# Optimization experiments

Measured on AMD Instinct MI355X. Metric: run time of the kernel, lower is better.

## Reference

```python
import jax, jax.numpy as jnp
import numpy as np

NUM_HEADS = 32
KV_HEADS = 8
HEAD_DIM = 64
HIDDEN = 2048
ROPE_THETA = 10000.0


def setup_inputs() -> dict:
    key = jax.random.key(0)
    ks = jax.random.split(key, 5)
    B, S, H = 2, 2048, HIDDEN
    scale = 0.02
    return {
        "x": jax.random.normal(ks[0], (B, S, H), dtype=jnp.float32),
        # weights stored as (in_features, out_features)
        "Wq": jax.random.normal(ks[1], (H, NUM_HEADS * HEAD_DIM), dtype=jnp.float32) * scale,
        "Wk": jax.random.normal(ks[2], (H, KV_HEADS * HEAD_DIM), dtype=jnp.float32) * scale,
        "Wv": jax.random.normal(ks[3], (H, KV_HEADS * HEAD_DIM), dtype=jnp.float32) * scale,
        "Wo": jax.random.normal(ks[4], (H, H), dtype=jnp.float32) * scale,
    }


def _rope_tables(seq_len, dtype):
    # freq over even dims, angles concatenated twice -> (S, HEAD_DIM)
    freq = 1.0 / (ROPE_THETA ** (jnp.arange(0, HEAD_DIM, 2, dtype=jnp.float32) / HEAD_DIM))
    ang = jnp.arange(seq_len, dtype=jnp.float32)[:, None] * freq[None, :]
    emb = jnp.concatenate([ang, ang], axis=-1)
    return jnp.cos(emb).astype(dtype), jnp.sin(emb).astype(dtype)


def _rotate_half(x):
    x1, x2 = jnp.split(x, 2, axis=-1)
    return jnp.concatenate([-x2, x1], axis=-1)


def reference(x, Wq, Wk, Wv, Wo):
    B, S, H = x.shape
    q = jnp.einsum("bsd,df->bsf", x, Wq).reshape(B, S, NUM_HEADS, HEAD_DIM).transpose(0, 2, 1, 3)
    k = jnp.einsum("bsd,df->bsf", x, Wk).reshape(B, S, KV_HEADS, HEAD_DIM).transpose(0, 2, 1, 3)
    v = jnp.einsum("bsd,df->bsf", x, Wv).reshape(B, S, KV_HEADS, HEAD_DIM).transpose(0, 2, 1, 3)

    cos, sin = _rope_tables(S, x.dtype)  # (S, HEAD_DIM), broadcasts over (B, h, S, D)
    q = q * cos + _rotate_half(q) * sin
    k = k * cos + _rotate_half(k) * sin

    n_rep = NUM_HEADS // KV_HEADS
    k = jnp.repeat(k, n_rep, axis=1)  # (B, NUM_HEADS, S, D)
    v = jnp.repeat(v, n_rep, axis=1)

    scores = jnp.einsum("bhsd,bhtd->bhst", q, k) / jnp.sqrt(jnp.asarray(HEAD_DIM, x.dtype))
    weights = jax.nn.softmax(scores, axis=-1)
    ctx = jnp.einsum("bhst,bhtd->bhsd", weights, v)
    ctx = ctx.transpose(0, 2, 1, 3).reshape(B, S, H)
    return jnp.einsum("bsd,df->bsf", ctx, Wo)
```

## Files before the change

kernel.cpp:

```cpp
#include <hip/hip_runtime.h>

typedef short s8v __attribute__((ext_vector_type(8)));
typedef int i2v __attribute__((ext_vector_type(2)));
typedef float f4v __attribute__((ext_vector_type(4)));

typedef const __attribute__((address_space(1))) char* gp1_t;
typedef __attribute__((address_space(3))) char* lp3_t;

__device__ __forceinline__ float bf2f(short s) {
    union { unsigned u; float f; } c;
    c.u = ((unsigned)(unsigned short)s) << 16;
    return c.f;
}
__device__ __forceinline__ short f2bf(float f) {
    union { float f; unsigned u; } c; c.f = f;
    unsigned r = (c.u + 0x7FFFu + ((c.u >> 16) & 1u)) >> 16;
    return (short)r;
}
__device__ __forceinline__ unsigned cvt_pk_bf16(float a, float b) {
    unsigned r;
    asm("v_cvt_pk_bf16_f32 %0, %1, %2" : "=v"(r) : "v"(a), "v"(b));
    return r;
}
__device__ __forceinline__ s8v cvt8(const float* __restrict__ p) {
    f4v a = *(const f4v*)p;
    f4v b = *(const f4v*)(p + 4);
    s8v r;
    r[0] = f2bf(a[0]); r[1] = f2bf(a[1]); r[2] = f2bf(a[2]); r[3] = f2bf(a[3]);
    r[4] = f2bf(b[0]); r[5] = f2bf(b[1]); r[6] = f2bf(b[2]); r[7] = f2bf(b[3]);
    return r;
}


__global__ __launch_bounds__(256) void cvt_x(const float* __restrict__ x,
                                             short* __restrict__ xb) {
    long i = ((long)blockIdx.x * 256 + threadIdx.x) * 8;
    *(s8v*)&xb[i] = cvt8(&x[i]);
}

__global__ __launch_bounds__(256) void cvt_wt(const float* __restrict__ W,
                                              short* __restrict__ Wt,
                                              int N, int obase) {
    __shared__ __align__(16) short tile[64 * 72];
    const int kt = blockIdx.y * 64, n0 = blockIdx.x * 64;
    const int t = threadIdx.x;
    const int r = t >> 4, c4 = (t & 15) * 4;
#pragma unroll
    for (int i = 0; i < 4; i++) {
        int kr = r + i * 16;
        f4v v = *(const f4v*)&W[(long)(kt + kr) * N + n0 + c4];
#pragma unroll
        for (int j = 0; j < 4; j++) tile[(c4 + j) * 72 + kr] = f2bf(v[j]);
    }
    __syncthreads();
    const int nr = t >> 3, kc = (t & 7) * 8;
#pragma unroll
    for (int i = 0; i < 2; i++) {
        int n = nr + i * 32;
        *(s8v*)&Wt[(long)(obase + n0 + n) * 2048 + kt + kc] = *(const s8v*)&tile[n * 72 + kc];
    }
}

template <bool CF32>
__global__ __launch_bounds__(256) void gemm_bt(const short* __restrict__ A,
                                               const short* __restrict__ Bt,
                                               void* __restrict__ Cv,
                                               int K, int lda, int ldb, int ldc) {
    __shared__ __align__(16) short As[128 * 32];
    __shared__ __align__(16) short Bs[128 * 32];
    const int tid = threadIdx.x;
    const int lane = tid & 63;
    const int wave = tid >> 6;
    const int quad = lane >> 4;
    const int l15 = lane & 15;
    const int m0 = blockIdx.y * 128;
    const int n0 = blockIdx.x * 128;
    const int wm = (wave & 1) * 64;
    const int wn = (wave >> 1) * 64;

    f4v acc[4][4];
#pragma unroll
    for (int i = 0; i < 4; i++)
#pragma unroll
        for (int j = 0; j < 4; j++) acc[i][j] = (f4v){0.f, 0.f, 0.f, 0.f};

    const int s0 = wave * 64 + lane, s1 = (4 + wave) * 64 + lane;
    const short* a0 = A + (long)(m0 + (s0 >> 2)) * lda + (s0 & 3) * 8;
    const short* a1 = A + (long)(m0 + (s1 >> 2)) * lda + (s1 & 3) * 8;
    const short* b0 = Bt + (long)(n0 + (s0 >> 2)) * ldb + (s0 & 3) * 8;
    const short* b1 = Bt + (long)(n0 + (s1 >> 2)) * ldb + (s1 & 3) * 8;
    char* lA0 = (char*)As + wave * 1024;
    char* lA1 = (char*)As + (4 + wave) * 1024;
    char* lB0 = (char*)Bs + wave * 1024;
    char* lB1 = (char*)Bs + (4 + wave) * 1024;

    for (int k0 = 0; k0 < K; k0 += 32) {
        __syncthreads();
        __builtin_amdgcn_global_load_lds((gp1_t)(a0 + k0), (lp3_t)lA0, 16, 0, 0);
        __builtin_amdgcn_global_load_lds((gp1_t)(a1 + k0), (lp3_t)lA1, 16, 0, 0);
        __builtin_amdgcn_global_load_lds((gp1_t)(b0 + k0), (lp3_t)lB0, 16, 0, 0);
        __builtin_amdgcn_global_load_lds((gp1_t)(b1 + k0), (lp3_t)lB1, 16, 0, 0);
        __syncthreads();
        s8v af[4], bfr[4];
#pragma unroll
        for (int mi = 0; mi < 4; mi++)
            af[mi] = *(const s8v*)(&As[(wm + mi * 16 + l15) * 32 + quad * 8]);
#pragma unroll
        for (int ni = 0; ni < 4; ni++)
            bfr[ni] = *(const s8v*)(&Bs[(wn + ni * 16 + l15) * 32 + quad * 8]);
#pragma unroll
        for (int mi = 0; mi < 4; mi++)
#pragma unroll
            for (int ni = 0; ni < 4; ni++)
                acc[mi][ni] = __builtin_amdgcn_mfma_f32_16x16x32_bf16(af[mi], bfr[ni], acc[mi][ni], 0, 0, 0);
    }
#pragma unroll
    for (int mi = 0; mi < 4; mi++)
#pragma unroll
        for (int ni = 0; ni < 4; ni++)
#pragma unroll
            for (int r = 0; r < 4; r++) {
                int row = m0 + wm + mi * 16 + quad * 4 + r;
                int col = n0 + wn + ni * 16 + l15;
                if (CF32) ((float*)Cv)[(long)row * ldc + col] = acc[mi][ni][r];
                else      ((short*)Cv)[(long)row * ldc + col] = f2bf(acc[mi][ni][r]);
            }
}

__global__ __launch_bounds__(256) void rope_kernel(short* __restrict__ qkv) {
    int tid = blockIdx.x * 256 + threadIdx.x;
    int p = tid % 1280;
    int row = tid / 1280;
    int head = p >> 5;
    int j = p & 31;
    int s = row & 2047;
    int c1 = head * 64 + j;
    float freq = exp2f(-(float)j * 0.4152410118609203f);
    float ang = (float)s * freq;
    float sn, cs;
    __sincosf(ang, &sn, &cs);
    long base = (long)row * 3072;
    float x1 = bf2f(qkv[base + c1]);
    float x2 = bf2f(qkv[base + c1 + 32]);
    qkv[base + c1]      = f2bf(x1 * cs - x2 * sn);
    qkv[base + c1 + 32] = f2bf(x2 * cs + x1 * sn);
}

__global__ __launch_bounds__(256) void vtrans(const short* __restrict__ qkv,
                                              short* __restrict__ Vt_g) {
    __shared__ __align__(16) short tile[64 * 72];
    const int kt = blockIdx.x * 64;
    const int kvh = blockIdx.y;
    const int b = blockIdx.z;
    const int t = threadIdx.x;
#pragma unroll
    for (int cc = 0; cc < 2; cc++) {
        int ch = t + cc * 256;
        int key = ch >> 3, d0 = (ch & 7) * 8;
        s8v v = *(const s8v*)&qkv[(long)(b * 2048 + kt + key) * 3072 + 2560 + kvh * 64 + d0];
#pragma unroll
        for (int i = 0; i < 8; i++) tile[(d0 + i) * 72 + key] = v[i];
    }
    __syncthreads();
#pragma unroll
    for (int cc = 0; cc < 2; cc++) {
        int ch = t + cc * 256;
        int d = ch >> 3, kc = (ch & 7) * 8;
        *(s8v*)&Vt_g[(long)((b * 8 + kvh) * 64 + d) * 2048 + kt + kc] = *(const s8v*)&tile[d * 72 + kc];
    }
}

__global__ __launch_bounds__(256, 3) void attn4(short* __restrict__ qkv,
                                                const short* __restrict__ Vt_g) {
    __shared__ __align__(16) short KV[2][2][4096];
    __shared__ __align__(16) short Ps[4][2][16 * 72];
    __shared__ float rsb[4][32];

    const int tid = threadIdx.x;
    const int lane = tid & 63;
    const int wave = tid >> 6;
    const int quad = lane >> 4;
    const int l15 = lane & 15;
    const int b = blockIdx.z;
    const int h = blockIdx.y;
    const int kvh = h >> 2;
    const int q0 = blockIdx.x * 128;

    const long kbase = ((long)b * 2048) * 3072 + 2048 + kvh * 64;
    const long vtbase = (long)(b * 8 + kvh) * 64 * 2048;

    const long qrow = (long)b * 2048 + q0 + wave * 32 + l15;
    const short* qp = qkv + qrow * 3072 + h * 64 + quad * 8;
    const s8v qf00 = *(const s8v*)(qp);
    const s8v qf01 = *(const s8v*)(qp + 32);
    const s8v qf10 = *(const s8v*)(qp + 16 * 3072);
    const s8v qf11 = *(const s8v*)(qp + 16 * 3072 + 32);

    const int rA = wave * 8 + (lane >> 3);
    const int sslot = (lane & 7) ^ (lane >> 3);
    const short* kA = qkv + kbase + (long)rA * 3072 + sslot * 8;
    const short* kB = kA + (long)32 * 3072;
    const short* vA = Vt_g + vtbase + (long)rA * 2048 + sslot * 8;
    const short* vB = vA + (long)32 * 2048;

    {
        char* kd = (char*)&KV[0][0][0] + wave * 1024;
        char* vd = (char*)&KV[0][1][0] + wave * 1024;
        __builtin_amdgcn_global_load_lds((gp1_t)kA, (lp3_t)kd, 16, 0, 0);
        __builtin_amdgcn_global_load_lds((gp1_t)kB, (lp3_t)(kd + 4096), 16, 0, 0);
        __builtin_amdgcn_global_load_lds((gp1_t)vA, (lp3_t)vd, 16, 0, 0);
        __builtin_amdgcn_global_load_lds((gp1_t)vB, (lp3_t)(vd + 4096), 16, 0, 0);
    }
    __syncthreads();

    const int ks0 = ((quad ^ (l15 & 7)) << 3);
    const int ks1 = ks0 ^ 32;

    const float CS = 0.18033688011112042f;

    float rs0 = 0.f, rs1 = 0.f;
    f4v o0[4], o1[4];
#pragma unroll
    for (int ni = 0; ni < 4; ni++) { o0[ni] = (f4v){0.f, 0.f, 0.f, 0.f}; o1[ni] = (f4v){0.f, 0.f, 0.f, 0.f}; }

    short* Pw0 = &Ps[wave][0][0];
    short* Pw1 = &Ps[wave][1][0];

    for (int t = 0; t < 32; ++t) {
        const short* Kb = &KV[t & 1][0][0];
        const short* Vb = &KV[t & 1][1][0];

        if (t < 31) {
            const long ko = (long)(t + 1) * (64 * 3072);
            const long vo = (long)(t + 1) * 64;
            char* kd = (char*)&KV[(t + 1) & 1][0][0] + wave * 1024;
            char* vd = (char*)&KV[(t + 1) & 1][1][0] + wave * 1024;
            __builtin_amdgcn_global_load_lds((gp1_t)(kA + ko), (lp3_t)kd, 16, 0, 0);
            __builtin_amdgcn_global_load_lds((gp1_t)(kB + ko), (lp3_t)(kd + 4096), 16, 0, 0);
            __builtin_amdgcn_global_load_lds((gp1_t)(vA + vo), (lp3_t)vd, 16, 0, 0);
            __builtin_amdgcn_global_load_lds((gp1_t)(vB + vo), (lp3_t)(vd + 4096), 16, 0, 0);
        }

#pragma unroll
        for (int ni = 0; ni < 4; ni++) {
            const int ro = (ni * 16 + l15) * 64;
            const s8v kf0 = *(const s8v*)&Kb[ro + ks0];
            const s8v kf1 = *(const s8v*)&Kb[ro + ks1];
            f4v a = (f4v){0.f, 0.f, 0.f, 0.f};
            a = __builtin_amdgcn_mfma_f32_16x16x32_bf16(kf0, qf00, a, 0, 0, 0);
            a = __builtin_amdgcn_mfma_f32_16x16x32_bf16(kf1, qf01, a, 0, 0, 0);
            {
                float p0 = exp2f(fmaf(a[0], CS, -24.f));
                float p1 = exp2f(fmaf(a[1], CS, -24.f));
                float p2 = exp2f(fmaf(a[2], CS, -24.f));
                float p3 = exp2f(fmaf(a[3], CS, -24.f));
                rs0 += (p0 + p1) + (p2 + p3);
                *(i2v*)&Pw0[l15 * 72 + ni * 16 + quad * 4] =
                    (i2v){(int)cvt_pk_bf16(p0, p1), (int)cvt_pk_bf16(p2, p3)};
            }
            f4v c = (f4v){0.f, 0.f, 0.f, 0.f};
            c = __builtin_amdgcn_mfma_f32_16x16x32_bf16(kf0, qf10, c, 0, 0, 0);
            c = __builtin_amdgcn_mfma_f32_16x16x32_bf16(kf1, qf11, c, 0, 0, 0);
            {
                float p0 = exp2f(fmaf(c[0], CS, -24.f));
                float p1 = exp2f(fmaf(c[1], CS, -24.f));
                float p2 = exp2f(fmaf(c[2], CS, -24.f));
                float p3 = exp2f(fmaf(c[3], CS, -24.f));
                rs1 += (p0 + p1) + (p2 + p3);
                *(i2v*)&Pw1[l15 * 72 + ni * 16 + quad * 4] =
                    (i2v){(int)cvt_pk_bf16(p0, p1), (int)cvt_pk_bf16(p2, p3)};
            }
        }

        const s8v pf00 = *(const s8v*)&Pw0[l15 * 72 + quad * 8];
        const s8v pf01 = *(const s8v*)&Pw0[l15 * 72 + 32 + quad * 8];
        const s8v pf10 = *(const s8v*)&Pw1[l15 * 72 + quad * 8];
        const s8v pf11 = *(const s8v*)&Pw1[l15 * 72 + 32 + quad * 8];
#pragma unroll
        for (int ni = 0; ni < 4; ni++) {
            const int ro = (ni * 16 + l15) * 64;
            const s8v vf0 = *(const s8v*)&Vb[ro + ks0];
            const s8v vf1 = *(const s8v*)&Vb[ro + ks1];
            o0[ni] = __builtin_amdgcn_mfma_f32_16x16x32_bf16(pf00, vf0, o0[ni], 0, 0, 0);
            o0[ni] = __builtin_amdgcn_mfma_f32_16x16x32_bf16(pf01, vf1, o0[ni], 0, 0, 0);
            o1[ni] = __builtin_amdgcn_mfma_f32_16x16x32_bf16(pf10, vf0, o1[ni], 0, 0, 0);
            o1[ni] = __builtin_amdgcn_mfma_f32_16x16x32_bf16(pf11, vf1, o1[ni], 0, 0, 0);
        }
        __syncthreads();
    }

    rs0 += __shfl_xor(rs0, 16); rs0 += __shfl_xor(rs0, 32);
    rs1 += __shfl_xor(rs1, 16); rs1 += __shfl_xor(rs1, 32);
    if (quad == 0) { rsb[wave][l15] = rs0; rsb[wave][16 + l15] = rs1; }
    __syncthreads();

#pragma unroll
    for (int r = 0; r < 4; r++) {
        const float i0 = 1.0f / rsb[wave][quad * 4 + r];
        const float i1 = 1.0f / rsb[wave][16 + quad * 4 + r];
        const long ob0 = ((long)b * 2048 + q0 + wave * 32 + quad * 4 + r) * 3072 + h * 64;
        const long ob1 = ob0 + 16 * 3072;
#pragma unroll
        for (int ni = 0; ni < 4; ni++) {
            qkv[ob0 + ni * 16 + l15] = f2bf(o0[ni][r] * i0);
            qkv[ob1 + ni * 16 + l15] = f2bf(o1[ni][r] * i1);
        }
    }
}


template <bool AF32, bool CF32>
__global__ __launch_bounds__(256) void gemm_bn(const void* __restrict__ Av,
                                               const float* __restrict__ B,
                                               void* __restrict__ Cv,
                                               int K, int N, int lda, int ldc) {
    __shared__ __align__(16) short As[128 * 40];
    __shared__ __align__(16) short Bs[128 * 40];
    const int tid = threadIdx.x;
    const int lane = tid & 63;
    const int wave = tid >> 6;
    const int quad = lane >> 4;
    const int l15 = lane & 15;
    const int m0 = blockIdx.y * 128;
    const int n0 = blockIdx.x * 128;
    const int wm = (wave & 1) * 64;
    const int wn = (wave >> 1) * 64;

    f4v acc[4][4];
#pragma unroll
    for (int i = 0; i < 4; i++)
#pragma unroll
        for (int j = 0; j < 4; j++) acc[i][j] = (f4v){0.f, 0.f, 0.f, 0.f};

    const int ar0 = tid >> 2, akc0 = (tid & 3) * 8;
    const int ar1 = (tid + 256) >> 2, akc1 = ((tid + 256) & 3) * 8;
    const int bk0 = tid >> 4, bnc0 = (tid & 15) * 8;
    const int bk1 = (tid + 256) >> 4, bnc1 = ((tid + 256) & 15) * 8;

    for (int k0 = 0; k0 < K; k0 += 32) {
        __syncthreads();
        if (AF32) {
            const float* A = (const float*)Av;
            *(s8v*)(&As[ar0 * 40 + akc0]) = cvt8(&A[(long)(m0 + ar0) * lda + k0 + akc0]);
            *(s8v*)(&As[ar1 * 40 + akc1]) = cvt8(&A[(long)(m0 + ar1) * lda + k0 + akc1]);
        } else {
            const short* A = (const short*)Av;
            *(s8v*)(&As[ar0 * 40 + akc0]) = *(const s8v*)(&A[(long)(m0 + ar0) * lda + k0 + akc0]);
            *(s8v*)(&As[ar1 * 40 + akc1]) = *(const s8v*)(&A[(long)(m0 + ar1) * lda + k0 + akc1]);
        }
        s8v b0 = cvt8(&B[(long)(k0 + bk0) * N + n0 + bnc0]);
        s8v b1 = cvt8(&B[(long)(k0 + bk1) * N + n0 + bnc1]);
#pragma unroll
        for (int i = 0; i < 8; i++) Bs[(bnc0 + i) * 40 + bk0] = b0[i];
#pragma unroll
        for (int i = 0; i < 8; i++) Bs[(bnc1 + i) * 40 + bk1] = b1[i];
        __syncthreads();
        s8v af[4], bfr[4];
#pragma unroll
        for (int mi = 0; mi < 4; mi++)
            af[mi] = *(const s8v*)(&As[(wm + mi * 16 + l15) * 40 + quad * 8]);
#pragma unroll
        for (int ni = 0; ni < 4; ni++)
            bfr[ni] = *(const s8v*)(&Bs[(wn + ni * 16 + l15) * 40 + quad * 8]);
#pragma unroll
        for (int mi = 0; mi < 4; mi++)
#pragma unroll
            for (int ni = 0; ni < 4; ni++)
                acc[mi][ni] = __builtin_amdgcn_mfma_f32_16x16x32_bf16(af[mi], bfr[ni], acc[mi][ni], 0, 0, 0);
    }
#pragma unroll
    for (int mi = 0; mi < 4; mi++)
#pragma unroll
        for (int ni = 0; ni < 4; ni++)
#pragma unroll
            for (int r = 0; r < 4; r++) {
                int row = m0 + wm + mi * 16 + quad * 4 + r;
                int col = n0 + wn + ni * 16 + l15;
                if (CF32) ((float*)Cv)[(long)row * ldc + col] = acc[mi][ni][r];
                else      ((short*)Cv)[(long)row * ldc + col] = f2bf(acc[mi][ni][r]);
            }
}

__global__ __launch_bounds__(256) void attn_kernel(short* __restrict__ qkv) {
    __shared__ __align__(16) short Qs[64 * 72];
    __shared__ __align__(16) short Ks[64 * 72];
    __shared__ __align__(16) short Vt[64 * 72];
    __shared__ __align__(16) short Ps[4][16 * 72];

    const int tid = threadIdx.x;
    const int lane = tid & 63;
    const int wave = tid >> 6;
    const int quad = lane >> 4;
    const int l15 = lane & 15;
    const int b = blockIdx.z;
    const int h = blockIdx.y;
    const int kvh = h >> 2;
    const int q0 = blockIdx.x * 64;

    const long qbase = ((long)b * 2048 + q0) * 3072 + h * 64;
    const long kbase = ((long)b * 2048) * 3072 + 2048 + kvh * 64;
    const long vbase = kbase + 512;

#pragma unroll
    for (int cc = 0; cc < 2; cc++) {
        int ch = tid + cc * 256;
        int r = ch >> 3, d0 = (ch & 7) * 8;
        *(s8v*)(&Qs[r * 72 + d0]) = *(const s8v*)(&qkv[qbase + (long)r * 3072 + d0]);
    }
    __syncthreads();
    s8v qf[2];
    qf[0] = *(const s8v*)(&Qs[(wave * 16 + l15) * 72 + quad * 8]);
    qf[1] = *(const s8v*)(&Qs[(wave * 16 + l15) * 72 + 32 + quad * 8]);

    float m_i[4], l_i[4];
    f4v o[4];
#pragma unroll
    for (int r = 0; r < 4; r++) { m_i[r] = -1e30f; l_i[r] = 0.0f; }
#pragma unroll
    for (int ni = 0; ni < 4; ni++) o[ni] = (f4v){0.f, 0.f, 0.f, 0.f};

    for (int kt = 0; kt < 2048; kt += 64) {
        __syncthreads();
#pragma unroll
        for (int cc = 0; cc < 2; cc++) {
            int ch = tid + cc * 256;
            int r = ch >> 3, d0 = (ch & 7) * 8;
            *(s8v*)(&Ks[r * 72 + d0]) = *(const s8v*)(&qkv[kbase + (long)(kt + r) * 3072 + d0]);
            s8v v = *(const s8v*)(&qkv[vbase + (long)(kt + r) * 3072 + d0]);
            int g = d0 >> 3;
            int chn = ((r >> 3) ^ g) * 8 + (r & 7);
#pragma unroll
            for (int i = 0; i < 8; i++) Vt[(d0 + i) * 72 + chn] = v[i];
        }
        __syncthreads();

        f4v sc[4];
#pragma unroll
        for (int ni = 0; ni < 4; ni++) {
            s8v kf0 = *(const s8v*)(&Ks[(ni * 16 + l15) * 72 + quad * 8]);
            s8v kf1 = *(const s8v*)(&Ks[(ni * 16 + l15) * 72 + 32 + quad * 8]);
            f4v a = (f4v){0.f, 0.f, 0.f, 0.f};
            a = __builtin_amdgcn_mfma_f32_16x16x32_bf16(qf[0], kf0, a, 0, 0, 0);
            a = __builtin_amdgcn_mfma_f32_16x16x32_bf16(qf[1], kf1, a, 0, 0, 0);
            sc[ni] = a * 0.125f;
        }
        float alpha[4], rs[4];
#pragma unroll
        for (int r = 0; r < 4; r++) {
            float v = fmaxf(fmaxf(sc[0][r], sc[1][r]), fmaxf(sc[2][r], sc[3][r]));
            v = fmaxf(v, __shfl_xor(v, 1));
            v = fmaxf(v, __shfl_xor(v, 2));
            v = fmaxf(v, __shfl_xor(v, 4));
            v = fmaxf(v, __shfl_xor(v, 8));
            float mn = fmaxf(m_i[r], v);
            alpha[r] = __expf(m_i[r] - mn);
            m_i[r] = mn;
            rs[r] = 0.f;
        }
#pragma unroll
        for (int ni = 0; ni < 4; ni++)
#pragma unroll
            for (int r = 0; r < 4; r++) {
                float pv = __expf(sc[ni][r] - m_i[r]);
                sc[ni][r] = pv;
                rs[r] += pv;
            }
#pragma unroll
        for (int r = 0; r < 4; r++) {
            float v = rs[r];
            v += __shfl_xor(v, 1);
            v += __shfl_xor(v, 2);
            v += __shfl_xor(v, 4);
            v += __shfl_xor(v, 8);
            l_i[r] = l_i[r] * alpha[r] + v;
        }
#pragma unroll
        for (int ni = 0; ni < 4; ni++)
#pragma unroll
            for (int r = 0; r < 4; r++) {
                int row = quad * 4 + r;
                int key = ni * 16 + l15;
                int chn = ((key >> 3) ^ (row >> 3)) * 8 + (key & 7);
                Ps[wave][row * 72 + chn] = f2bf(sc[ni][r]);
            }
        __syncthreads();
#pragma unroll
        for (int ni = 0; ni < 4; ni++) {
            f4v t = o[ni];
            t[0] *= alpha[0]; t[1] *= alpha[1]; t[2] *= alpha[2]; t[3] *= alpha[3];
            o[ni] = t;
        }
        s8v pf0 = *(const s8v*)(&Ps[wave][l15 * 72 + ((quad ^ (l15 >> 3)) * 8)]);
        s8v pf1 = *(const s8v*)(&Ps[wave][l15 * 72 + (((4 + quad) ^ (l15 >> 3)) * 8)]);
#pragma unroll
        for (int ni = 0; ni < 4; ni++) {
            int d = ni * 16 + l15;
            s8v vf0 = *(const s8v*)(&Vt[d * 72 + ((quad ^ (d >> 3)) * 8)]);
            s8v vf1 = *(const s8v*)(&Vt[d * 72 + (((4 + quad) ^ (d >> 3)) * 8)]);
            o[ni] = __builtin_amdgcn_mfma_f32_16x16x32_bf16(pf0, vf0, o[ni], 0, 0, 0);
            o[ni] = __builtin_amdgcn_mfma_f32_16x16x32_bf16(pf1, vf1, o[ni], 0, 0, 0);
        }
    }
#pragma unroll
    for (int r = 0; r < 4; r++) {
        float inv = 1.0f / l_i[r];
        int srow = q0 + wave * 16 + quad * 4 + r;
        long obase = ((long)b * 2048 + srow) * 3072 + h * 64;
#pragma unroll
        for (int ni = 0; ni < 4; ni++)
            qkv[obase + ni * 16 + l15] = f2bf(o[ni][r] * inv);
    }
}

extern "C" void kernel_launch(void* const* d_in, const int* in_sizes, int n_in,
                              void* d_out, int out_size, void* d_ws, size_t ws_size,
                              hipStream_t stream) {
    (void)in_sizes; (void)n_in; (void)out_size;
    const float* x  = (const float*)d_in[0];
    const float* Wq = (const float*)d_in[1];
    const float* Wk = (const float*)d_in[2];
    const float* Wv = (const float*)d_in[3];
    const float* Wo = (const float*)d_in[4];

    const size_t need = 67108864ULL;
    if (ws_size >= need) {
        short* xb    = (short*)d_ws;
        short* Wqkvt = xb + 8388608;
        short* Wot   = Wqkvt + 6291456;
        short* qkv   = Wot + 4194304;
        short* Vt_g  = qkv + 12582912;

        cvt_x<<<4096, 256, 0, stream>>>(x, xb);
        cvt_wt<<<dim3(32, 32), 256, 0, stream>>>(Wq, Wqkvt, 2048, 0);
        cvt_wt<<<dim3(8, 32), 256, 0, stream>>>(Wk, Wqkvt, 512, 2048);
        cvt_wt<<<dim3(8, 32), 256, 0, stream>>>(Wv, Wqkvt, 512, 2560);
        cvt_wt<<<dim3(32, 32), 256, 0, stream>>>(Wo, Wot, 2048, 0);
        gemm_bt<false><<<dim3(24, 32), 256, 0, stream>>>(xb, Wqkvt, qkv, 2048, 2048, 2048, 3072);
        rope_kernel<<<dim3(20480), 256, 0, stream>>>(qkv);
        vtrans<<<dim3(32, 8, 2), 256, 0, stream>>>(qkv, Vt_g);
        attn4<<<dim3(16, 32, 2), 256, 0, stream>>>(qkv, Vt_g);
        gemm_bt<true><<<dim3(16, 32), 256, 0, stream>>>(qkv, Wot, d_out, 2048, 3072, 2048, 2048);
    } else {
        short* qkv = (short*)d_ws;
        gemm_bn<true, false><<<dim3(16, 32), 256, 0, stream>>>(x, Wq, qkv,        2048, 2048, 2048, 3072);
        gemm_bn<true, false><<<dim3(4, 32), 256, 0, stream>>>(x, Wk, qkv + 2048, 2048,  512, 2048, 3072);
        gemm_bn<true, false><<<dim3(4, 32), 256, 0, stream>>>(x, Wv, qkv + 2560, 2048,  512, 2048, 3072);
        rope_kernel<<<dim3(20480), 256, 0, stream>>>(qkv);
        attn_kernel<<<dim3(32, 32, 2), 256, 0, stream>>>(qkv);
        gemm_bn<false, true><<<dim3(16, 32), 256, 0, stream>>>(qkv, Wo, d_out, 2048, 2048, 3072, 2048);
    }
}
```

Measured before the change: 376.0 us.

## Fold softmax scale into Wk, remap workgroups for XCD locality, pack row sums

The softmax scale (log2e/sqrt(d)) is folded into the K weight during bf16 conversion, and the -24 offset is used as the MFMA accumulator's initial value, which removes the per-element FMA before exp2. Workgroup indices in the GEMM and attention kernels are remapped so that consecutive blocks sharing operands land on the same XCD, for better L2 reuse. Row-sum accumulation uses packed float2 adds. Scaling K before bf16 rounding slightly changes numerics, and RoPE now operates on pre-scaled K, which is still correct because RoPE is linear.

```diff
diff --git a/kernel.cpp b/kernel.cpp
--- a/kernel.cpp
+++ b/kernel.cpp
@@ -2,6 +2,7 @@
 
 typedef short s8v __attribute__((ext_vector_type(8)));
 typedef int i2v __attribute__((ext_vector_type(2)));
+typedef float f2v __attribute__((ext_vector_type(2)));
 typedef float f4v __attribute__((ext_vector_type(4)));
 
 typedef const __attribute__((address_space(1))) char* gp1_t;
@@ -40,7 +41,7 @@
 
 __global__ __launch_bounds__(256) void cvt_wt(const float* __restrict__ W,
                                               short* __restrict__ Wt,
-                                              int N, int obase) {
+                                              int N, int obase, float scale) {
     __shared__ __align__(16) short tile[64 * 72];
     const int kt = blockIdx.y * 64, n0 = blockIdx.x * 64;
     const int t = threadIdx.x;
@@ -50,7 +51,7 @@
         int kr = r + i * 16;
         f4v v = *(const f4v*)&W[(long)(kt + kr) * N + n0 + c4];
 #pragma unroll
-        for (int j = 0; j < 4; j++) tile[(c4 + j) * 72 + kr] = f2bf(v[j]);
+        for (int j = 0; j < 4; j++) tile[(c4 + j) * 72 + kr] = f2bf(v[j] * scale);
     }
     __syncthreads();
     const int nr = t >> 3, kc = (t & 7) * 8;
@@ -73,8 +74,13 @@
     const int wave = tid >> 6;
     const int quad = lane >> 4;
     const int l15 = lane & 15;
-    const int m0 = blockIdx.y * 128;
-    const int n0 = blockIdx.x * 128;
+
+    const int nwg = gridDim.x * gridDim.y;
+    int f = blockIdx.y * gridDim.x + blockIdx.x;
+    if ((nwg & 7) == 0) f = (f & 7) * (nwg >> 3) + (f >> 3);
+    const int m0 = (f / gridDim.x) * 128;
+    const int n0 = (f % gridDim.x) * 128;
+
     const int wm = (wave & 1) * 64;
     const int wn = (wave >> 1) * 64;
 
@@ -181,10 +187,13 @@
     const int wave = tid >> 6;
     const int quad = lane >> 4;
     const int l15 = lane & 15;
-    const int b = blockIdx.z;
-    const int h = blockIdx.y;
+
+    int f = (blockIdx.z * 32 + blockIdx.y) * 16 + blockIdx.x;
+    f = (f & 7) * 128 + (f >> 3);
+    const int b = f >> 9;
+    const int h = (f >> 4) & 31;
     const int kvh = h >> 2;
-    const int q0 = blockIdx.x * 128;
+    const int q0 = (f & 15) * 128;
 
     const long kbase = ((long)b * 2048) * 3072 + 2048 + kvh * 64;
     const long vtbase = (long)(b * 8 + kvh) * 64 * 2048;
@@ -216,9 +225,7 @@
     const int ks0 = ((quad ^ (l15 & 7)) << 3);
     const int ks1 = ks0 ^ 32;
 
-    const float CS = 0.18033688011112042f;
-
-    float rs0 = 0.f, rs1 = 0.f;
+    f2v rs0v = (f2v){0.f, 0.f}, rs1v = (f2v){0.f, 0.f};
     f4v o0[4], o1[4];
 #pragma unroll
     for (int ni = 0; ni < 4; ni++) { o0[ni] = (f4v){0.f, 0.f, 0.f, 0.f}; o1[ni] = (f4v){0.f, 0.f, 0.f, 0.f}; }
@@ -246,27 +253,29 @@
             const int ro = (ni * 16 + l15) * 64;
             const s8v kf0 = *(const s8v*)&Kb[ro + ks0];
             const s8v kf1 = *(const s8v*)&Kb[ro + ks1];
-            f4v a = (f4v){0.f, 0.f, 0.f, 0.f};
+            f4v a = (f4v){-24.f, -24.f, -24.f, -24.f};
             a = __builtin_amdgcn_mfma_f32_16x16x32_bf16(kf0, qf00, a, 0, 0, 0);
             a = __builtin_amdgcn_mfma_f32_16x16x32_bf16(kf1, qf01, a, 0, 0, 0);
             {
-                float p0 = exp2f(fmaf(a[0], CS, -24.f));
-                float p1 = exp2f(fmaf(a[1], CS, -24.f));
-                float p2 = exp2f(fmaf(a[2], CS, -24.f));
-                float p3 = exp2f(fmaf(a[3], CS, -24.f));
-                rs0 += (p0 + p1) + (p2 + p3);
+                float p0 = exp2f(a[0]);
+                float p1 = exp2f(a[1]);
+                float p2 = exp2f(a[2]);
+                float p3 = exp2f(a[3]);
+                rs0v += (f2v){p0, p1};
+                rs0v += (f2v){p2, p3};
                 *(i2v*)&Pw0[l15 * 72 + ni * 16 + quad * 4] =
                     (i2v){(int)cvt_pk_bf16(p0, p1), (int)cvt_pk_bf16(p2, p3)};
             }
-            f4v c = (f4v){0.f, 0.f, 0.f, 0.f};
+            f4v c = (f4v){-24.f, -24.f, -24.f, -24.f};
             c = __builtin_amdgcn_mfma_f32_16x16x32_bf16(kf0, qf10, c, 0, 0, 0);
             c = __builtin_amdgcn_mfma_f32_16x16x32_bf16(kf1, qf11, c, 0, 0, 0);
             {
-                float p0 = exp2f(fmaf(c[0], CS, -24.f));
-                float p1 = exp2f(fmaf(c[1], CS, -24.f));
-                float p2 = exp2f(fmaf(c[2], CS, -24.f));
-                float p3 = exp2f(fmaf(c[3], CS, -24.f));
-                rs1 += (p0 + p1) + (p2 + p3);
+                float p0 = exp2f(c[0]);
+                float p1 = exp2f(c[1]);
+                float p2 = exp2f(c[2]);
+                float p3 = exp2f(c[3]);
+                rs1v += (f2v){p0, p1};
+                rs1v += (f2v){p2, p3};
                 *(i2v*)&Pw1[l15 * 72 + ni * 16 + quad * 4] =
                     (i2v){(int)cvt_pk_bf16(p0, p1), (int)cvt_pk_bf16(p2, p3)};
             }
@@ -289,6 +298,8 @@
         __syncthreads();
     }
 
+    float rs0 = rs0v[0] + rs0v[1];
+    float rs1 = rs1v[0] + rs1v[1];
     rs0 += __shfl_xor(rs0, 16); rs0 += __shfl_xor(rs0, 32);
     rs1 += __shfl_xor(rs1, 16); rs1 += __shfl_xor(rs1, 32);
     if (quad == 0) { rsb[wave][l15] = rs0; rsb[wave][16 + l15] = rs1; }
@@ -522,6 +533,7 @@
     const float* Wv = (const float*)d_in[3];
     const float* Wo = (const float*)d_in[4];
 
+    const float CS = 0.18033688011112042f;
     const size_t need = 67108864ULL;
     if (ws_size >= need) {
         short* xb    = (short*)d_ws;
@@ -531,10 +543,10 @@
         short* Vt_g  = qkv + 12582912;
 
         cvt_x<<<4096, 256, 0, stream>>>(x, xb);
-        cvt_wt<<<dim3(32, 32), 256, 0, stream>>>(Wq, Wqkvt, 2048, 0);
-        cvt_wt<<<dim3(8, 32), 256, 0, stream>>>(Wk, Wqkvt, 512, 2048);
-        cvt_wt<<<dim3(8, 32), 256, 0, stream>>>(Wv, Wqkvt, 512, 2560);
-        cvt_wt<<<dim3(32, 32), 256, 0, stream>>>(Wo, Wot, 2048, 0);
+        cvt_wt<<<dim3(32, 32), 256, 0, stream>>>(Wq, Wqkvt, 2048, 0, 1.0f);
+        cvt_wt<<<dim3(8, 32), 256, 0, stream>>>(Wk, Wqkvt, 512, 2048, CS);
+        cvt_wt<<<dim3(8, 32), 256, 0, stream>>>(Wv, Wqkvt, 512, 2560, 1.0f);
+        cvt_wt<<<dim3(32, 32), 256, 0, stream>>>(Wo, Wot, 2048, 0, 1.0f);
         gemm_bt<false><<<dim3(24, 32), 256, 0, stream>>>(xb, Wqkvt, qkv, 2048, 2048, 2048, 3072);
         rope_kernel<<<dim3(20480), 256, 0, stream>>>(qkv);
         vtrans<<<dim3(32, 8, 2), 256, 0, stream>>>(qkv, Vt_g);
```

New measurement: 364.7 us. 1.03x faster.
